# Kernel tuning notes

Hardware: AMD Instinct MI355X
Metric: run time of the kernel (lower is better)

## Reference

```python
import jax, jax.numpy as jnp
import numpy as np

N, E, D_IN, H, D = 170000, 1200000, 128, 4, 32
NEG_SLOPE = 0.2


def setup_inputs() -> dict:
    key = jax.random.key(0)
    ks = jax.random.split(key, 8)
    x = jax.random.normal(ks[0], (N, D_IN), dtype=jnp.float32)
    # xavier-normal-ish scale for linear weights
    W_embed = jax.random.normal(ks[1], (D_IN, H * D), dtype=jnp.float32) * (2.0 / (D_IN + H * D)) ** 0.5
    a_src = jax.random.normal(ks[2], (H, D), dtype=jnp.float32) * (2.0 / (1 + H * D)) ** 0.5
    a_dst = jax.random.normal(ks[3], (H, D), dtype=jnp.float32) * (2.0 / (1 + H * D)) ** 0.5
    W_lin = jax.random.normal(ks[4], (D_IN, H * D), dtype=jnp.float32) * (2.0 / (D_IN + H * D)) ** 0.5
    bias = jnp.zeros((H * D,), dtype=jnp.float32)
    src = jax.random.randint(ks[5], (E,), 0, N, dtype=jnp.int32)
    dst = jax.random.randint(ks[6], (E,), 0, N, dtype=jnp.int32)
    return {"x": x, "W_embed": W_embed, "a_src": a_src, "a_dst": a_dst,
            "W_lin": W_lin, "bias": bias, "src": src, "dst": dst}


def reference(x, W_embed, a_src, a_dst, W_lin, bias, src, dst):
    n = x.shape[0]
    # node projections: [N, H, D]
    h = (x @ W_embed).reshape(n, H, D)
    dot_src = jnp.einsum('nhd,hd->nh', h, a_src)  # [N, H]
    dot_dst = jnp.einsum('nhd,hd->nh', h, a_dst)  # [N, H]
    # edge attention logits: leaky_relu(dot_src[u] + dot_dst[v])  [E, H]
    z = dot_src[src] + dot_dst[dst]
    logit = jnp.where(z >= 0, z, NEG_SLOPE * z)
    # edge softmax over incoming edges of each destination node
    m = jax.ops.segment_max(logit, dst, num_segments=n)          # [N, H]
    e = jnp.exp(logit - m[dst])                                   # [E, H]
    denom = jax.ops.segment_sum(e, dst, num_segments=n)          # [N, H]
    prob = e / denom[dst]                                         # [E, H]
    # weighted scatter-sum aggregation: sum_e prob_e * h[src_e]
    msg = h[src] * prob[:, :, None]                               # [E, H, D]
    out = jax.ops.segment_sum(msg, dst, num_segments=n)          # [N, H, D]
    out = out.reshape(n, H * D)
    out = out + x @ W_lin
    out = out + bias[None, :]
    return out
```

## Files before the change

### kernel.cpp

```cpp
#include <hip/hip_runtime.h>
#include <hip/hip_bf16.h>

static constexpr int   N_NODES   = 170000;
static constexpr int   E_EDGES   = 1200000;
static constexpr float NEG_SLOPE = 0.2f;

typedef __attribute__((ext_vector_type(8))) short bfrag8;
typedef __attribute__((ext_vector_type(4))) float facc4;

__device__ __forceinline__ short f2bf(float f) {
    __hip_bfloat16 h = __float2bfloat16(f);
    return *reinterpret_cast<short*>(&h);
}

__global__ void wt_init_kernel(const float* __restrict__ We,
                               const float* __restrict__ Wl,
                               const float* __restrict__ a_src,
                               const float* __restrict__ a_dst,
                               short* __restrict__ WtG,
                               int* __restrict__ deg)
{
    const int t = threadIdx.x;
    if (blockIdx.x < 128) {
        const int k = blockIdx.x;
        if (t < 128) WtG[t * 128 + k] = f2bf(We[k * 128 + t]);
        else         WtG[t * 128 + k] = f2bf(Wl[k * 128 + (t - 128)]);
    } else if (blockIdx.x < 136) {
        const int idx = (blockIdx.x - 128) * 256 + t;
        if (idx < 1024) {
            const int g = idx >> 7;
            const int k = idx & 127;
            const int hh = g & 3;
            const float* av = (g < 4) ? a_src : a_dst;
            float s = 0.f;
            #pragma unroll
            for (int d = 0; d < 32; ++d)
                s += We[k * 128 + hh * 32 + d] * av[hh * 32 + d];
            WtG[(256 + g) * 128 + k] = f2bf(s);
        } else {
            const int z = idx - 1024;
            WtG[(264 + (z >> 7)) * 128 + (z & 127)] = 0;
        }
    }
    const int i = blockIdx.x * 256 + t;
    if (i < N_NODES) deg[i] = 0;
}

__global__ void hist_kernel(const int* __restrict__ dst,
                            int* __restrict__ deg,
                            int* __restrict__ seq)
{
    int e = blockIdx.x * blockDim.x + threadIdx.x;
    if (e < E_EDGES) {
        const int s = atomicAdd(&deg[dst[e]], 1);
        __builtin_nontemporal_store(s, &seq[e]);
    }
}

__global__ __launch_bounds__(256) void scan_local_kernel(
    const int* __restrict__ deg, int* __restrict__ row_ptr, int* __restrict__ bsum)
{
    __shared__ int sh[256];
    const int t = threadIdx.x;
    const int base = blockIdx.x * 1024 + t * 4;
    int v0 = (base + 0 < N_NODES) ? deg[base + 0] : 0;
    int v1 = (base + 1 < N_NODES) ? deg[base + 1] : 0;
    int v2 = (base + 2 < N_NODES) ? deg[base + 2] : 0;
    int v3 = (base + 3 < N_NODES) ? deg[base + 3] : 0;
    const int tot = v0 + v1 + v2 + v3;
    sh[t] = tot;
    __syncthreads();
    for (int off = 1; off < 256; off <<= 1) {
        int add = (t >= off) ? sh[t - off] : 0;
        __syncthreads();
        sh[t] += add;
        __syncthreads();
    }
    const int excl = sh[t] - tot;
    if (base + 0 < N_NODES) row_ptr[base + 0] = excl;
    if (base + 1 < N_NODES) row_ptr[base + 1] = excl + v0;
    if (base + 2 < N_NODES) row_ptr[base + 2] = excl + v0 + v1;
    if (base + 3 < N_NODES) row_ptr[base + 3] = excl + v0 + v1 + v2;
    if (t == 255) bsum[blockIdx.x] = sh[255];
}

__global__ __launch_bounds__(256) void scan_add_kernel(
    int* __restrict__ row_ptr, const int* __restrict__ bsum)
{
    const int t   = threadIdx.x;
    const int blk = blockIdx.x;
    int v = (t < blk) ? bsum[t] : 0;
    #pragma unroll
    for (int m = 32; m >= 1; m >>= 1) v += __shfl_xor(v, m, 64);
    __shared__ int sh[4];
    if ((t & 63) == 0) sh[t >> 6] = v;
    __syncthreads();
    const int boff = sh[0] + sh[1] + sh[2] + sh[3];

    const int base = blk * 1024 + t * 4;
    #pragma unroll
    for (int q = 0; q < 4; ++q)
        if (base + q < N_NODES) row_ptr[base + q] += boff;
    if (blk == 0 && t == 0) row_ptr[N_NODES] = E_EDGES;
}

__global__ void csr_place_kernel(const int* __restrict__ src,
                                 const int* __restrict__ dst,
                                 const int* __restrict__ seq,
                                 const int* __restrict__ rowp,
                                 int* __restrict__ srcs)
{
    int e = blockIdx.x * blockDim.x + threadIdx.x;
    if (e >= E_EDGES) return;
    const int p = rowp[dst[e]] + seq[e];
    __builtin_nontemporal_store(src[e], &srcs[p]);
}

static constexpr int LDB = 136;

#define LOAD_A_FRAGS                                                         \
    long ar0 = row0 + w * 32 + col;                                          \
    long ar1 = ar0 + 16;                                                     \
    if (ar0 > N_NODES - 1) ar0 = N_NODES - 1;                                \
    if (ar1 > N_NODES - 1) ar1 = N_NODES - 1;                                \
    const float4* xp0 = (const float4*)&x[ar0 * 128 + quad * 8];             \
    const float4* xp1 = (const float4*)&x[ar1 * 128 + quad * 8];             \
    float4 av[2][4][2];                                                      \
    _Pragma("unroll")                                                        \
    for (int ks = 0; ks < 4; ++ks) {                                         \
        av[0][ks][0] = xp0[ks * 8 + 0];                                      \
        av[0][ks][1] = xp0[ks * 8 + 1];                                      \
        av[1][ks][0] = xp1[ks * 8 + 0];                                      \
        av[1][ks][1] = xp1[ks * 8 + 1];                                      \
    }

#define CONVERT_A_FRAGS                                                      \
    bfrag8 afr[2][4];                                                        \
    _Pragma("unroll")                                                        \
    for (int m = 0; m < 2; ++m)                                              \
        _Pragma("unroll")                                                    \
        for (int ks = 0; ks < 4; ++ks) {                                     \
            bfrag8 tv;                                                       \
            tv[0] = f2bf(av[m][ks][0].x); tv[1] = f2bf(av[m][ks][0].y);      \
            tv[2] = f2bf(av[m][ks][0].z); tv[3] = f2bf(av[m][ks][0].w);      \
            tv[4] = f2bf(av[m][ks][1].x); tv[5] = f2bf(av[m][ks][1].y);      \
            tv[6] = f2bf(av[m][ks][1].z); tv[7] = f2bf(av[m][ks][1].w);      \
            afr[m][ks] = tv;                                                 \
        }

__global__ __launch_bounds__(256, 4) void embed_gemm_kernel(
    const float* __restrict__ x,
    const short* __restrict__ WtG,
    short* __restrict__ hbuf,
    float* __restrict__ dsrc,
    float* __restrict__ ddst)
{
    __shared__ short Bs[144 * LDB];
    const int tid  = threadIdx.x;
    const long row0 = (long)blockIdx.x * 128;
    const int w    = tid >> 6;
    const int l    = tid & 63;
    const int col  = l & 15;
    const int quad = l >> 4;

    LOAD_A_FRAGS

    #pragma unroll
    for (int it = 0; it < 9; ++it) {
        const int idx = it * 256 + tid;
        const int n   = idx >> 4;
        const int kc  = (idx & 15) * 8;
        const int gn  = (n < 128) ? n : (n + 128);
        *(int4*)&Bs[n * LDB + kc] = *(const int4*)&WtG[gn * 128 + kc];
    }

    CONVERT_A_FRAGS
    __syncthreads();

    facc4 acc[2][8];
    facc4 adot[2];
    #pragma unroll
    for (int m = 0; m < 2; ++m) {
        adot[m] = (facc4)(0.f);
        #pragma unroll
        for (int t = 0; t < 8; ++t) acc[m][t] = (facc4)(0.f);
    }

    #pragma unroll
    for (int ks = 0; ks < 4; ++ks) {
        #pragma unroll
        for (int t = 0; t < 8; ++t) {
            const bfrag8 b = *(const bfrag8*)&Bs[(t * 16 + col) * LDB + ks * 32 + quad * 8];
            acc[0][t] = __builtin_amdgcn_mfma_f32_16x16x32_bf16(afr[0][ks], b, acc[0][t], 0, 0, 0);
            acc[1][t] = __builtin_amdgcn_mfma_f32_16x16x32_bf16(afr[1][ks], b, acc[1][t], 0, 0, 0);
        }
        const bfrag8 bd = *(const bfrag8*)&Bs[(128 + col) * LDB + ks * 32 + quad * 8];
        adot[0] = __builtin_amdgcn_mfma_f32_16x16x32_bf16(afr[0][ks], bd, adot[0], 0, 0, 0);
        adot[1] = __builtin_amdgcn_mfma_f32_16x16x32_bf16(afr[1][ks], bd, adot[1], 0, 0, 0);
    }

    #pragma unroll
    for (int m = 0; m < 2; ++m) {
        const long rbase = row0 + w * 32 + m * 16 + quad * 4;
        #pragma unroll
        for (int r = 0; r < 4; ++r) {
            const long mm = rbase + r;
            if (mm >= N_NODES) continue;
            #pragma unroll
            for (int t = 0; t < 8; ++t)
                hbuf[mm * 128 + t * 16 + col] = f2bf(acc[m][t][r]);
            if (col < 4)      dsrc[mm * 4 + col]       = adot[m][r];
            else if (col < 8) ddst[mm * 4 + (col - 4)] = adot[m][r];
        }
    }
}

__global__ __launch_bounds__(256, 4) void lin_gemm_kernel(
    const float* __restrict__ x,
    const short* __restrict__ WtG,
    const float* __restrict__ bias,
    float* __restrict__ outp)
{
    __shared__ short Bs[128 * LDB];
    const int tid  = threadIdx.x;
    const long row0 = (long)blockIdx.x * 128;
    const int w    = tid >> 6;
    const int l    = tid & 63;
    const int col  = l & 15;
    const int quad = l >> 4;

    LOAD_A_FRAGS

    #pragma unroll
    for (int it = 0; it < 8; ++it) {
        const int idx = it * 256 + tid;
        const int n   = idx >> 4;
        const int kc  = (idx & 15) * 8;
        *(int4*)&Bs[n * LDB + kc] = *(const int4*)&WtG[(128 + n) * 128 + kc];
    }

    CONVERT_A_FRAGS
    __syncthreads();

    facc4 acc[2][8];
    #pragma unroll
    for (int m = 0; m < 2; ++m)
        #pragma unroll
        for (int t = 0; t < 8; ++t) acc[m][t] = (facc4)(0.f);

    #pragma unroll
    for (int ks = 0; ks < 4; ++ks) {
        #pragma unroll
        for (int t = 0; t < 8; ++t) {
            const bfrag8 b = *(const bfrag8*)&Bs[(t * 16 + col) * LDB + ks * 32 + quad * 8];
            acc[0][t] = __builtin_amdgcn_mfma_f32_16x16x32_bf16(afr[0][ks], b, acc[0][t], 0, 0, 0);
            acc[1][t] = __builtin_amdgcn_mfma_f32_16x16x32_bf16(afr[1][ks], b, acc[1][t], 0, 0, 0);
        }
    }

    #pragma unroll
    for (int t = 0; t < 8; ++t) {
        const float bv = bias[t * 16 + col];
        #pragma unroll
        for (int m = 0; m < 2; ++m) {
            const long rbase = row0 + w * 32 + m * 16 + quad * 4;
            #pragma unroll
            for (int r = 0; r < 4; ++r) {
                const long mm = rbase + r;
                if (mm < N_NODES) outp[mm * 128 + t * 16 + col] = acc[m][t][r] + bv;
            }
        }
    }
}

__global__ __launch_bounds__(256) void agg_kernel(
    const int* __restrict__ row_ptr, const int* __restrict__ srcs,
    const float* __restrict__ dsrc, const float* __restrict__ ddst,
    const short* __restrict__ hbuf, float* __restrict__ outp)
{
    const long node = (long)blockIdx.x * 4 + (threadIdx.x >> 6);
    if (node >= N_NODES) return;
    const int lane   = threadIdx.x & 63;
    const int head_c = lane >> 4;
    const int c2     = lane << 1;
    const int slot   = lane >> 2;
    const int head_w = lane & 3;
    const int start = __builtin_amdgcn_readfirstlane(row_ptr[node]);
    const int end   = __builtin_amdgcn_readfirstlane(row_ptr[node + 1]);
    if (start == end) return;

    const float ddw = ddst[node * 4 + head_w];

    float a0 = 0.f, a1 = 0.f, dn = 0.f;

#define EDGE_BODY(i) \
    const float w##i = __shfl(wv, (k + i) * 4 + head_c); \
    const int   s##i = __builtin_amdgcn_readlane(sv, (k + i) * 4); \
    const uint  h##i = *(const uint*)&hbuf[(long)s##i * 128 + c2];

#define EDGE_ACC(i) { \
    dn += w##i; \
    a0 = fmaf(w##i, __uint_as_float(h##i << 16),         a0); \
    a1 = fmaf(w##i, __uint_as_float(h##i & 0xFFFF0000u), a1); }

    for (int j = start; j < end; j += 16) {
        const int idx = j + slot;
        const int ci  = (idx < end) ? idx : (end - 1);
        const int sv  = srcs[ci];
        float z = dsrc[sv * 4 + head_w] + ddw;
        z = fmaxf(z, NEG_SLOPE * z);
        float wv = __expf(z);
        if (idx >= end) wv = 0.f;
        const int chunk = (end - j < 16) ? (end - j) : 16;
        for (int k = 0; k < chunk; k += 4) {
            EDGE_BODY(0) EDGE_BODY(1) EDGE_BODY(2) EDGE_BODY(3)
            EDGE_ACC(0) EDGE_ACC(1) EDGE_ACC(2) EDGE_ACC(3)
        }
    }
#undef EDGE_BODY
#undef EDGE_ACC

    const float inv = 1.f / dn;
    float2* op = (float2*)&outp[node * 128 + c2];
    float2 o = *op;
    o.x += a0 * inv;
    o.y += a1 * inv;
    *op = o;
}

extern "C" void kernel_launch(void* const* d_in, const int* in_sizes, int n_in,
                              void* d_out, int out_size, void* d_ws, size_t ws_size,
                              hipStream_t stream)
{
    const float* x       = (const float*)d_in[0];
    const float* W_embed = (const float*)d_in[1];
    const float* a_src   = (const float*)d_in[2];
    const float* a_dst   = (const float*)d_in[3];
    const float* W_lin   = (const float*)d_in[4];
    const float* bias    = (const float*)d_in[5];
    const int*   src     = (const int*)d_in[6];
    const int*   dst     = (const int*)d_in[7];
    float* outp = (float*)d_out;

    char* ws = (char*)d_ws;
    short* WtG   = (short*)ws;  ws += (size_t)272 * 128 * sizeof(short);
    short* hbuf  = (short*)ws;  ws += (size_t)N_NODES * 128 * sizeof(short);
    int*   srcs  = (int*)ws;    ws += (size_t)E_EDGES * sizeof(int);
    float* dsrc  = (float*)ws;  ws += (size_t)N_NODES * 4 * sizeof(float);
    float* ddst  = (float*)ws;  ws += (size_t)N_NODES * 4 * sizeof(float);
    int*   deg   = (int*)ws;    ws += (size_t)N_NODES * sizeof(int);
    int*   rowp  = (int*)ws;    ws += (size_t)(N_NODES + 16) * sizeof(int);
    int*   bsum  = (int*)ws;    ws += 256 * sizeof(int);

    int* seq = (int*)dsrc;

    const int SCAN_BLKS = (N_NODES + 1023) / 1024;

    wt_init_kernel<<<(N_NODES + 255) / 256, 256, 0, stream>>>(
        W_embed, W_lin, a_src, a_dst, WtG, deg);
    hist_kernel<<<(E_EDGES + 255) / 256, 256, 0, stream>>>(dst, deg, seq);
    scan_local_kernel<<<SCAN_BLKS, 256, 0, stream>>>(deg, rowp, bsum);
    scan_add_kernel<<<SCAN_BLKS, 256, 0, stream>>>(rowp, bsum);

    csr_place_kernel<<<(E_EDGES + 255) / 256, 256, 0, stream>>>(
        src, dst, seq, rowp, srcs);

    lin_gemm_kernel<<<(N_NODES + 127) / 128, 256, 0, stream>>>(
        x, WtG, bias, outp);
    embed_gemm_kernel<<<(N_NODES + 127) / 128, 256, 0, stream>>>(
        x, WtG, hbuf, dsrc, ddst);

    agg_kernel<<<(N_NODES + 3) / 4, 256, 0, stream>>>(
        rowp, srcs, dsrc, ddst, hbuf, outp);
}
```

Measured before the change: 402.8 us.

## Use 512-thread GEMM blocks with 16 rows per wave; unroll aggregation and split launch

The embed and linear GEMM kernels now launch 512 threads per block, so each wave handles 16 rows instead of 32. This halves accumulator registers and spreads the shared weight-tile load across more threads. The aggregation kernel's edge loop is unrolled by 8 instead of 4, the output load is hoisted ahead of the edge loop, and the aggregation is split into two launches over node halves. The changes aim for more latency hiding and occupancy, at the cost of more work per block on the shared weight tile and an extra kernel launch.

```diff
diff --git a/kernel.cpp b/kernel.cpp
--- a/kernel.cpp
+++ b/kernel.cpp
@@ -118,37 +118,30 @@
 
 static constexpr int LDB = 136;
 
-#define LOAD_A_FRAGS                                                         \
-    long ar0 = row0 + w * 32 + col;                                          \
-    long ar1 = ar0 + 16;                                                     \
-    if (ar0 > N_NODES - 1) ar0 = N_NODES - 1;                                \
-    if (ar1 > N_NODES - 1) ar1 = N_NODES - 1;                                \
-    const float4* xp0 = (const float4*)&x[ar0 * 128 + quad * 8];             \
-    const float4* xp1 = (const float4*)&x[ar1 * 128 + quad * 8];             \
-    float4 av[2][4][2];                                                      \
+#define LOAD_A_FRAGS_16                                                      \
+    long ar = row0 + w * 16 + col;                                           \
+    if (ar > N_NODES - 1) ar = N_NODES - 1;                                  \
+    const float4* xp = (const float4*)&x[ar * 128 + quad * 8];               \
+    float4 av[4][2];                                                         \
     _Pragma("unroll")                                                        \
     for (int ks = 0; ks < 4; ++ks) {                                         \
-        av[0][ks][0] = xp0[ks * 8 + 0];                                      \
-        av[0][ks][1] = xp0[ks * 8 + 1];                                      \
-        av[1][ks][0] = xp1[ks * 8 + 0];                                      \
-        av[1][ks][1] = xp1[ks * 8 + 1];                                      \
-    }
-
-#define CONVERT_A_FRAGS                                                      \
-    bfrag8 afr[2][4];                                                        \
+        av[ks][0] = xp[ks * 8 + 0];                                          \
+        av[ks][1] = xp[ks * 8 + 1];                                          \
+    }
+
+#define CONVERT_A_FRAGS_16                                                   \
+    bfrag8 afr[4];                                                           \
     _Pragma("unroll")                                                        \
-    for (int m = 0; m < 2; ++m)                                              \
-        _Pragma("unroll")                                                    \
-        for (int ks = 0; ks < 4; ++ks) {                                     \
-            bfrag8 tv;                                                       \
-            tv[0] = f2bf(av[m][ks][0].x); tv[1] = f2bf(av[m][ks][0].y);      \
-            tv[2] = f2bf(av[m][ks][0].z); tv[3] = f2bf(av[m][ks][0].w);      \
-            tv[4] = f2bf(av[m][ks][1].x); tv[5] = f2bf(av[m][ks][1].y);      \
-            tv[6] = f2bf(av[m][ks][1].z); tv[7] = f2bf(av[m][ks][1].w);      \
-            afr[m][ks] = tv;                                                 \
-        }
-
-__global__ __launch_bounds__(256, 4) void embed_gemm_kernel(
+    for (int ks = 0; ks < 4; ++ks) {                                         \
+        bfrag8 tv;                                                           \
+        tv[0] = f2bf(av[ks][0].x); tv[1] = f2bf(av[ks][0].y);                \
+        tv[2] = f2bf(av[ks][0].z); tv[3] = f2bf(av[ks][0].w);                \
+        tv[4] = f2bf(av[ks][1].x); tv[5] = f2bf(av[ks][1].y);                \
+        tv[6] = f2bf(av[ks][1].z); tv[7] = f2bf(av[ks][1].w);                \
+        afr[ks] = tv;                                                        \
+    }
+
+__global__ __launch_bounds__(512, 4) void embed_gemm_kernel(
     const float* __restrict__ x,
     const short* __restrict__ WtG,
     short* __restrict__ hbuf,
@@ -163,59 +156,52 @@
     const int col  = l & 15;
     const int quad = l >> 4;
 
-    LOAD_A_FRAGS
-
-    #pragma unroll
-    for (int it = 0; it < 9; ++it) {
-        const int idx = it * 256 + tid;
-        const int n   = idx >> 4;
-        const int kc  = (idx & 15) * 8;
-        const int gn  = (n < 128) ? n : (n + 128);
-        *(int4*)&Bs[n * LDB + kc] = *(const int4*)&WtG[gn * 128 + kc];
-    }
-
-    CONVERT_A_FRAGS
+    LOAD_A_FRAGS_16
+
+    #pragma unroll
+    for (int it = 0; it < 5; ++it) {
+        const int idx = it * 512 + tid;
+        if (idx < 2304) {
+            const int n   = idx >> 4;
+            const int kc  = (idx & 15) * 8;
+            const int gn  = (n < 128) ? n : (n + 128);
+            *(int4*)&Bs[n * LDB + kc] = *(const int4*)&WtG[gn * 128 + kc];
+        }
+    }
+
+    CONVERT_A_FRAGS_16
     __syncthreads();
 
-    facc4 acc[2][8];
-    facc4 adot[2];
-    #pragma unroll
-    for (int m = 0; m < 2; ++m) {
-        adot[m] = (facc4)(0.f);
-        #pragma unroll
-        for (int t = 0; t < 8; ++t) acc[m][t] = (facc4)(0.f);
-    }
+    facc4 acc[8];
+    facc4 adot = (facc4)(0.f);
+    #pragma unroll
+    for (int t = 0; t < 8; ++t) acc[t] = (facc4)(0.f);
 
     #pragma unroll
     for (int ks = 0; ks < 4; ++ks) {
         #pragma unroll
         for (int t = 0; t < 8; ++t) {
             const bfrag8 b = *(const bfrag8*)&Bs[(t * 16 + col) * LDB + ks * 32 + quad * 8];
-            acc[0][t] = __builtin_amdgcn_mfma_f32_16x16x32_bf16(afr[0][ks], b, acc[0][t], 0, 0, 0);
-            acc[1][t] = __builtin_amdgcn_mfma_f32_16x16x32_bf16(afr[1][ks], b, acc[1][t], 0, 0, 0);
+            acc[t] = __builtin_amdgcn_mfma_f32_16x16x32_bf16(afr[ks], b, acc[t], 0, 0, 0);
         }
         const bfrag8 bd = *(const bfrag8*)&Bs[(128 + col) * LDB + ks * 32 + quad * 8];
-        adot[0] = __builtin_amdgcn_mfma_f32_16x16x32_bf16(afr[0][ks], bd, adot[0], 0, 0, 0);
-        adot[1] = __builtin_amdgcn_mfma_f32_16x16x32_bf16(afr[1][ks], bd, adot[1], 0, 0, 0);
-    }
-
-    #pragma unroll
-    for (int m = 0; m < 2; ++m) {
-        const long rbase = row0 + w * 32 + m * 16 + quad * 4;
+        adot = __builtin_amdgcn_mfma_f32_16x16x32_bf16(afr[ks], bd, adot, 0, 0, 0);
+    }
+
+    const long rbase = row0 + w * 16 + quad * 4;
+    #pragma unroll
+    for (int r = 0; r < 4; ++r) {
+        const long mm = rbase + r;
+        if (mm >= N_NODES) continue;
         #pragma unroll
-        for (int r = 0; r < 4; ++r) {
-            const long mm = rbase + r;
-            if (mm >= N_NODES) continue;
-            #pragma unroll
-            for (int t = 0; t < 8; ++t)
-                hbuf[mm * 128 + t * 16 + col] = f2bf(acc[m][t][r]);
-            if (col < 4)      dsrc[mm * 4 + col]       = adot[m][r];
-            else if (col < 8) ddst[mm * 4 + (col - 4)] = adot[m][r];
-        }
-    }
-}
-
-__global__ __launch_bounds__(256, 4) void lin_gemm_kernel(
+        for (int t = 0; t < 8; ++t)
+            hbuf[mm * 128 + t * 16 + col] = f2bf(acc[t][r]);
+        if (col < 4)      dsrc[mm * 4 + col]       = adot[r];
+        else if (col < 8) ddst[mm * 4 + (col - 4)] = adot[r];
+    }
+}
+
+__global__ __launch_bounds__(512, 4) void lin_gemm_kernel(
     const float* __restrict__ x,
     const short* __restrict__ WtG,
     const float* __restrict__ bias,
@@ -229,46 +215,40 @@
     const int col  = l & 15;
     const int quad = l >> 4;
 
-    LOAD_A_FRAGS
-
-    #pragma unroll
-    for (int it = 0; it < 8; ++it) {
-        const int idx = it * 256 + tid;
+    LOAD_A_FRAGS_16
+
+    #pragma unroll
+    for (int it = 0; it < 4; ++it) {
+        const int idx = it * 512 + tid;
         const int n   = idx >> 4;
         const int kc  = (idx & 15) * 8;
         *(int4*)&Bs[n * LDB + kc] = *(const int4*)&WtG[(128 + n) * 128 + kc];
     }
 
-    CONVERT_A_FRAGS
+    CONVERT_A_FRAGS_16
     __syncthreads();
 
-    facc4 acc[2][8];
-    #pragma unroll
-    for (int m = 0; m < 2; ++m)
-        #pragma unroll
-        for (int t = 0; t < 8; ++t) acc[m][t] = (facc4)(0.f);
+    facc4 acc[8];
+    #pragma unroll
+    for (int t = 0; t < 8; ++t) acc[t] = (facc4)(0.f);
 
     #pragma unroll
     for (int ks = 0; ks < 4; ++ks) {
         #pragma unroll
         for (int t = 0; t < 8; ++t) {
             const bfrag8 b = *(const bfrag8*)&Bs[(t * 16 + col) * LDB + ks * 32 + quad * 8];
-            acc[0][t] = __builtin_amdgcn_mfma_f32_16x16x32_bf16(afr[0][ks], b, acc[0][t], 0, 0, 0);
-            acc[1][t] = __builtin_amdgcn_mfma_f32_16x16x32_bf16(afr[1][ks], b, acc[1][t], 0, 0, 0);
-        }
-    }
-
+            acc[t] = __builtin_amdgcn_mfma_f32_16x16x32_bf16(afr[ks], b, acc[t], 0, 0, 0);
+        }
+    }
+
+    const long rbase = row0 + w * 16 + quad * 4;
     #pragma unroll
     for (int t = 0; t < 8; ++t) {
         const float bv = bias[t * 16 + col];
         #pragma unroll
-        for (int m = 0; m < 2; ++m) {
-            const long rbase = row0 + w * 32 + m * 16 + quad * 4;
-            #pragma unroll
-            for (int r = 0; r < 4; ++r) {
-                const long mm = rbase + r;
-                if (mm < N_NODES) outp[mm * 128 + t * 16 + col] = acc[m][t][r] + bv;
-            }
+        for (int r = 0; r < 4; ++r) {
+            const long mm = rbase + r;
+            if (mm < N_NODES) outp[mm * 128 + t * 16 + col] = acc[t][r] + bv;
         }
     }
 }
@@ -276,9 +256,10 @@
 __global__ __launch_bounds__(256) void agg_kernel(
     const int* __restrict__ row_ptr, const int* __restrict__ srcs,
     const float* __restrict__ dsrc, const float* __restrict__ ddst,
-    const short* __restrict__ hbuf, float* __restrict__ outp)
-{
-    const long node = (long)blockIdx.x * 4 + (threadIdx.x >> 6);
+    const short* __restrict__ hbuf, float* __restrict__ outp,
+    int node0)
+{
+    const long node = (long)node0 + blockIdx.x * 4 + (threadIdx.x >> 6);
     if (node >= N_NODES) return;
     const int lane   = threadIdx.x & 63;
     const int head_c = lane >> 4;
@@ -289,6 +270,8 @@
     const int end   = __builtin_amdgcn_readfirstlane(row_ptr[node + 1]);
     if (start == end) return;
 
+    float2* op = (float2*)&outp[node * 128 + c2];
+    float2 o = *op;
     const float ddw = ddst[node * 4 + head_w];
 
     float a0 = 0.f, a1 = 0.f, dn = 0.f;
@@ -312,17 +295,17 @@
         float wv = __expf(z);
         if (idx >= end) wv = 0.f;
         const int chunk = (end - j < 16) ? (end - j) : 16;
-        for (int k = 0; k < chunk; k += 4) {
+        for (int k = 0; k < chunk; k += 8) {
             EDGE_BODY(0) EDGE_BODY(1) EDGE_BODY(2) EDGE_BODY(3)
+            EDGE_BODY(4) EDGE_BODY(5) EDGE_BODY(6) EDGE_BODY(7)
             EDGE_ACC(0) EDGE_ACC(1) EDGE_ACC(2) EDGE_ACC(3)
+            EDGE_ACC(4) EDGE_ACC(5) EDGE_ACC(6) EDGE_ACC(7)
         }
     }
 #undef EDGE_BODY
 #undef EDGE_ACC
 
     const float inv = 1.f / dn;
-    float2* op = (float2*)&outp[node * 128 + c2];
-    float2 o = *op;
     o.x += a0 * inv;
     o.y += a1 * inv;
     *op = o;
@@ -355,6 +338,7 @@
     int* seq = (int*)dsrc;
 
     const int SCAN_BLKS = (N_NODES + 1023) / 1024;
+    const int HALF_N    = 85000;
 
     wt_init_kernel<<<(N_NODES + 255) / 256, 256, 0, stream>>>(
         W_embed, W_lin, a_src, a_dst, WtG, deg);
@@ -365,11 +349,13 @@
     csr_place_kernel<<<(E_EDGES + 255) / 256, 256, 0, stream>>>(
         src, dst, seq, rowp, srcs);
 
-    lin_gemm_kernel<<<(N_NODES + 127) / 128, 256, 0, stream>>>(
+    lin_gemm_kernel<<<(N_NODES + 127) / 128, 512, 0, stream>>>(
         x, WtG, bias, outp);
-    embed_gemm_kernel<<<(N_NODES + 127) / 128, 256, 0, stream>>>(
+    embed_gemm_kernel<<<(N_NODES + 127) / 128, 512, 0, stream>>>(
         x, WtG, hbuf, dsrc, ddst);
 
-    agg_kernel<<<(N_NODES + 3) / 4, 256, 0, stream>>>(
-        rowp, srcs, dsrc, ddst, hbuf, outp);
-}
+    agg_kernel<<<HALF_N / 4, 256, 0, stream>>>(
+        rowp, srcs, dsrc, ddst, hbuf, outp, 0);
+    agg_kernel<<<(N_NODES - HALF_N + 3) / 4, 256, 0, stream>>>(
+        rowp, srcs, dsrc, ddst, hbuf, outp, HALF_N);
+}
```

Result: faster. 393.9 us (-2.2%).
